# Kernel tuning notes

Hardware: AMD Instinct MI355X
Metric: run time of the kernel (lower is better)

## Reference

```python
import jax, jax.numpy as jnp
import numpy as np

B, T, F, H1, H2 = 16384, 10, 500, 256, 100  # batch, seq_len, noise_dim/seq_len, LSTM units, GRU units


def setup_inputs() -> dict:
    key = jax.random.key(0)
    ks = jax.random.split(key, 10)
    s = 0.02  # small init so relu activations stay bounded over time steps
    return {
        "noise": jax.random.normal(ks[0], (B, T * F), dtype=jnp.float32),
        "Wx_lstm": jax.random.normal(ks[1], (F, 4 * H1), dtype=jnp.float32) * s,
        "Wh_lstm": jax.random.normal(ks[2], (H1, 4 * H1), dtype=jnp.float32) * s,
        "b_lstm": jnp.zeros((4 * H1,), dtype=jnp.float32),
        "Wx_gru": jax.random.normal(ks[3], (H1, 3 * H2), dtype=jnp.float32) * s,
        "Wh_gru": jax.random.normal(ks[4], (H2, 3 * H2), dtype=jnp.float32) * s,
        "b_in_gru": jnp.zeros((3 * H2,), dtype=jnp.float32),
        "b_rec_gru": jnp.zeros((3 * H2,), dtype=jnp.float32),
        "Wd": jax.random.normal(ks[5], (H2, T), dtype=jnp.float32) * s,
        "bd": jnp.zeros((T,), dtype=jnp.float32),
    }


def _lstm(x, Wx, Wh, b):
    # x: [T, B, F]; Keras LSTM with activation='relu', recurrent_activation='sigmoid'
    Bn = x.shape[1]
    H = Wh.shape[0]
    def step(carry, x_t):
        h, c = carry
        z = x_t @ Wx + h @ Wh + b  # [B, 4H]
        i, f, g, o = jnp.split(z, 4, axis=-1)  # Keras gate order: i, f, c, o
        i = jax.nn.sigmoid(i)
        f = jax.nn.sigmoid(f)
        g = jax.nn.relu(g)
        o = jax.nn.sigmoid(o)
        c = f * c + i * g
        h = o * jax.nn.relu(c)
        return (h, c), h
    h0 = jnp.zeros((Bn, H), dtype=x.dtype)
    (_, _), hs = jax.lax.scan(step, (h0, h0), x)
    return hs  # [T, B, H]


def _gru(x, Wx, Wh, b_in, b_rec):
    # x: [T, B, H1]; Keras GRU (reset_after=True) with activation='relu'
    Bn = x.shape[1]
    H = Wh.shape[0]
    def step(h, x_t):
        mx = x_t @ Wx + b_in    # [B, 3H]
        mh = h @ Wh + b_rec     # [B, 3H]
        xz, xr, xh = jnp.split(mx, 3, axis=-1)  # Keras gate order: z, r, h
        hz, hr, hh = jnp.split(mh, 3, axis=-1)
        z = jax.nn.sigmoid(xz + hz)
        r = jax.nn.sigmoid(xr + hr)
        hcand = jax.nn.relu(xh + r * hh)
        h = z * h + (1.0 - z) * hcand
        return h, None
    h0 = jnp.zeros((Bn, H), dtype=x.dtype)
    h_final, _ = jax.lax.scan(step, h0, x)
    return h_final  # [B, H]


def reference(noise, Wx_lstm, Wh_lstm, b_lstm, Wx_gru, Wh_gru, b_in_gru, b_rec_gru, Wd, bd):
    Fdim = Wx_lstm.shape[0]
    Tdim = noise.shape[1] // Fdim
    x = noise.reshape(noise.shape[0], Tdim, Fdim)      # Reshape((T, F))
    x = jnp.transpose(x, (1, 0, 2))                    # [T, B, F] for scan
    hs = _lstm(x, Wx_lstm, Wh_lstm, b_lstm)            # [T, B, 256]
    h = _gru(hs, Wx_gru, Wh_gru, b_in_gru, b_rec_gru)  # [B, 100]
    return jax.nn.relu(h @ Wd + bd)                    # [B, T]
```

## Files before the change

### kernel.cpp

```cpp
#include <hip/hip_runtime.h>

#define Bsz 16384
#define TT 10
#define FF 500
#define H1c 256
#define H2c 100

typedef _Float16 half8 __attribute__((ext_vector_type(8)));
typedef float floatx4 __attribute__((ext_vector_type(4)));

__device__ __forceinline__ float sigm(float x) { return 1.0f / (1.0f + __expf(-x)); }

#define GLOAD16(g, l) __builtin_amdgcn_global_load_lds( \
    (const __attribute__((address_space(1))) void*)(g), \
    (__attribute__((address_space(3))) void*)(l), 16, 0, 0)

__global__ __launch_bounds__(256)
void conv_all(const float* __restrict__ noise, _Float16* __restrict__ xc)
{
    const int idx = blockIdx.x * 256 + threadIdx.x;
    const int rb = idx >> 6;
    const int kc = (idx & 63) << 3;
    const int b = rb / 10;
    const int t = rb - b * 10;
    const float* src = noise + (size_t)rb * FF + kc;
    half8 v;
    if (kc + 8 <= FF) {
        float4 u0 = *(const float4*)src;
        float4 u1 = *(const float4*)(src + 4);
        v[0] = (_Float16)u0.x; v[1] = (_Float16)u0.y; v[2] = (_Float16)u0.z; v[3] = (_Float16)u0.w;
        v[4] = (_Float16)u1.x; v[5] = (_Float16)u1.y; v[6] = (_Float16)u1.z; v[7] = (_Float16)u1.w;
    } else {
        #pragma unroll
        for (int j = 0; j < 8; ++j)
            v[j] = (kc + j < FF) ? (_Float16)src[j] : (_Float16)0.f;
    }
    *(half8*)(xc + ((size_t)t * Bsz + b) * 512 + kc) = v;
}

__global__ __launch_bounds__(256)
void prep_lstm_w(const float* __restrict__ Wx, const float* __restrict__ Wh,
                 _Float16* __restrict__ WT)
{
    const int idx = blockIdx.x * 256 + threadIdx.x;
    const int np = idx / 768, k = idx % 768;
    const int A2 = np >> 8, B2 = (np >> 6) & 3, g = (np >> 4) & 3, u = np & 15;
    const int U = A2 * 64 + B2 * 16 + u;
    const int col = g * 256 + U;
    float v = 0.f;
    if (k < 512) { if (k < FF) v = Wx[(size_t)k * 1024 + col]; }
    else v = Wh[(size_t)(k - 512) * 1024 + col];
    WT[idx] = (_Float16)v;
}

__global__ __launch_bounds__(256)
void prep_gru_w(const float* __restrict__ Wxg, const float* __restrict__ Whg,
                _Float16* __restrict__ WT)
{
    const int idx = blockIdx.x * 256 + threadIdx.x;
    if (idx >= 384 * 384) return;
    const int np = idx / 384, k = idx % 384;
    const int nb = np / 96, rem = np % 96;
    const int wxx = rem / 48, g = (rem % 48) / 16, u = rem & 15;
    const int U = nb * 32 + wxx * 16 + u;
    float v = 0.f;
    if (U < H2c) {
        if (k < 256) v = Wxg[(size_t)k * 300 + g * H2c + U];
        else if (k - 256 < H2c) v = Whg[(size_t)(k - 256) * 300 + g * H2c + U];
    }
    WT[idx] = (_Float16)v;
}

__device__ __forceinline__
void lstm_tile(int bid, const _Float16* __restrict__ xct, const _Float16* __restrict__ WT,
               const float* __restrict__ bias,
               const _Float16* __restrict__ h_prev, const float* __restrict__ c_prev,
               _Float16* __restrict__ h_out, float* __restrict__ c_out,
               int first, _Float16* smem)
{
    _Float16* As = smem;
    _Float16* Bs = smem + 32768;

    const int tid = threadIdx.x;
    const int lane = tid & 63;
    const int w = tid >> 6;
    const int wy = w >> 2, wx = w & 3;
    const int xcd = bid & 7;
    const int nb = xcd >> 1;
    const int row0 = (((xcd & 1) << 5) + (bid >> 3)) * 256;

    const int fr = lane & 15;
    const int l4 = lane >> 4;
    const int sr8 = lane >> 3;
    const int qsrc = (((lane & 7) ^ (sr8 & 7)) << 3);

    floatx4 acc[8][4];
    #pragma unroll
    for (int a = 0; a < 8; ++a)
        #pragma unroll
        for (int b = 0; b < 4; ++b) acc[a][b] = (floatx4){0.f, 0.f, 0.f, 0.f};

    const int nkt = first ? 8 : 12;

    #pragma unroll
    for (int q = 0; q < 4; ++q) {
        const int r = q * 64 + w * 8;
        GLOAD16(xct + (size_t)(row0 + r + sr8) * 512 + qsrc, &As[r * 64]);
        GLOAD16(WT + (size_t)(nb * 256 + r + sr8) * 768 + qsrc, &Bs[r * 64]);
    }
    __syncthreads();

    for (int T = 0; T < nkt; ++T) {
        const int pbase = (T & 1) * 16384;
        const int sbase = pbase ^ 16384;
        const int kb2 = (T + 1) * 64;
        const bool do_stage = (T + 1 < nkt);
        const bool from_x = kb2 < 512;

        half8 af[4][2], bf[2][2];

        auto LOAD_AF = [&](int mh) {
            #pragma unroll
            for (int j = 0; j < 4; ++j) {
                const int row = wy * 128 + (mh * 4 + j) * 16 + fr;
                #pragma unroll
                for (int ks = 0; ks < 2; ++ks) {
                    const int ch = (ks * 4 + l4) ^ (fr & 7);
                    af[j][ks] = *(const half8*)&As[pbase + row * 64 + ch * 8];
                }
            }
        };
        auto LOAD_BF = [&](int nh) {
            #pragma unroll
            for (int jn = 0; jn < 2; ++jn) {
                const int row = wx * 64 + (nh * 2 + jn) * 16 + fr;
                #pragma unroll
                for (int ks = 0; ks < 2; ++ks) {
                    const int ch = (ks * 4 + l4) ^ (fr & 7);
                    bf[jn][ks] = *(const half8*)&Bs[pbase + row * 64 + ch * 8];
                }
            }
        };
        auto STAGE_Q = [&](int q) {
            const int r = q * 64 + w * 8;
            if (from_x)
                GLOAD16(xct + (size_t)(row0 + r + sr8) * 512 + kb2 + qsrc, &As[sbase + r * 64]);
            else
                GLOAD16(h_prev + (size_t)(row0 + r + sr8) * 256 + (kb2 - 512) + qsrc, &As[sbase + r * 64]);
            GLOAD16(WT + (size_t)(nb * 256 + r + sr8) * 768 + kb2 + qsrc, &Bs[sbase + r * 64]);
        };
        auto MFMA_Q = [&](int mh, int nh) {
            __builtin_amdgcn_s_setprio(1);
            #pragma unroll
            for (int ks = 0; ks < 2; ++ks)
                #pragma unroll
                for (int j = 0; j < 4; ++j)
                    #pragma unroll
                    for (int jn = 0; jn < 2; ++jn)
                        acc[mh * 4 + j][nh * 2 + jn] = __builtin_amdgcn_mfma_f32_16x16x32_f16(
                            af[j][ks], bf[jn][ks], acc[mh * 4 + j][nh * 2 + jn], 0, 0, 0);
            __builtin_amdgcn_s_setprio(0);
        };

        LOAD_AF(0); LOAD_BF(0);
        if (do_stage) { STAGE_Q(0); STAGE_Q(1); }
        MFMA_Q(0, 0);
        LOAD_BF(1);
        if (do_stage) { STAGE_Q(2); STAGE_Q(3); }
        MFMA_Q(0, 1);
        LOAD_AF(1);
        MFMA_Q(1, 1);
        LOAD_BF(0);
        MFMA_Q(1, 0);
        __syncthreads();
    }

    const int U = nb * 64 + wx * 16 + fr;
    const float bi = bias[0 * 256 + U];
    const float bff = bias[1 * 256 + U];
    const float bg = bias[2 * 256 + U];
    const float bo = bias[3 * 256 + U];
    const int rbase = row0 + wy * 128 + l4 * 4;
    #pragma unroll
    for (int mi = 0; mi < 8; ++mi) {
        #pragma unroll
        for (int r = 0; r < 4; ++r) {
            const int row = rbase + mi * 16 + r;
            const float cp = first ? 0.f : c_prev[(size_t)row * 256 + U];
            const float zi = acc[mi][0][r] + bi;
            const float zf = acc[mi][1][r] + bff;
            const float zg = acc[mi][2][r] + bg;
            const float zo = acc[mi][3][r] + bo;
            const float ig = sigm(zi), fg = sigm(zf), og = sigm(zo);
            const float gg = fmaxf(zg, 0.f);
            const float cv = fg * cp + ig * gg;
            const float hv = og * fmaxf(cv, 0.f);
            c_out[(size_t)row * 256 + U] = cv;
            h_out[(size_t)row * 256 + U] = (_Float16)hv;
        }
    }
}

__device__ __forceinline__
void gru_tile(int bid, int first,
              const _Float16* __restrict__ h_r, const _Float16* __restrict__ g16_r,
              const _Float16* __restrict__ WTg,
              const float* __restrict__ b_in, const float* __restrict__ b_rec,
              _Float16* __restrict__ g16_w,
              _Float16* As, _Float16* Bs)
{
    const int tid = threadIdx.x;
    const int lane = tid & 63;
    const int w = tid >> 6;
    const int wq = w >> 2;
    const int wn = w & 3;
    const int rb0 = bid * 64;
    const int fr = lane & 15;
    const int l4 = lane >> 4;
    const int sr8 = lane >> 3;
    const int qsrc = (((lane & 7) ^ sr8) << 3);

    floatx4 accA[2][6], accB[2][6];
    #pragma unroll
    for (int a = 0; a < 2; ++a)
        #pragma unroll
        for (int b = 0; b < 6; ++b) {
            accA[a][b] = (floatx4){0.f, 0.f, 0.f, 0.f};
            accB[a][b] = (floatx4){0.f, 0.f, 0.f, 0.f};
        }

    const int nkt = first ? 4 : 6;
    for (int kt = 0; kt < nkt; ++kt) {
        const int kb = kt * 64;
        {
            const int r = w * 8;
            if (kt < 4)
                GLOAD16(h_r + (size_t)(rb0 + r + sr8) * 256 + kb + qsrc, &As[r * 64]);
            else
                GLOAD16(g16_r + (size_t)(rb0 + r + sr8) * 128 + (kb - 256) + qsrc, &As[r * 64]);
        }
        #pragma unroll
        for (int q = 0; q < 6; ++q) {
            const int r = q * 64 + w * 8;
            GLOAD16(WTg + (size_t)(r + sr8) * 384 + kb + qsrc, &Bs[r * 64]);
        }
        __syncthreads();
        #pragma unroll
        for (int ks = 0; ks < 2; ++ks) {
            half8 af[2], bf[6];
            const int ch0 = (ks * 4 + l4) ^ (fr & 7);
            #pragma unroll
            for (int mf = 0; mf < 2; ++mf) {
                const int row = wq * 32 + mf * 16 + fr;
                af[mf] = *(const half8*)&As[row * 64 + ch0 * 8];
            }
            #pragma unroll
            for (int nf = 0; nf < 6; ++nf) {
                const int row = wn * 96 + nf * 16 + fr;
                bf[nf] = *(const half8*)&Bs[row * 64 + ch0 * 8];
            }
            if (kt < 4) {
                #pragma unroll
                for (int mf = 0; mf < 2; ++mf)
                    #pragma unroll
                    for (int nf = 0; nf < 6; ++nf)
                        accA[mf][nf] = __builtin_amdgcn_mfma_f32_16x16x32_f16(af[mf], bf[nf], accA[mf][nf], 0, 0, 0);
            } else {
                #pragma unroll
                for (int mf = 0; mf < 2; ++mf)
                    #pragma unroll
                    for (int nf = 0; nf < 6; ++nf)
                        accB[mf][nf] = __builtin_amdgcn_mfma_f32_16x16x32_f16(af[mf], bf[nf], accB[mf][nf], 0, 0, 0);
            }
        }
        __syncthreads();
    }

    #pragma unroll
    for (int mf = 0; mf < 2; ++mf) {
        #pragma unroll
        for (int wxx = 0; wxx < 2; ++wxx) {
            const int U = wn * 32 + wxx * 16 + fr;
            const bool uv = U < H2c;
            const float bzi = uv ? b_in[U] : 0.f;
            const float bri = uv ? b_in[H2c + U] : 0.f;
            const float bhi = uv ? b_in[2 * H2c + U] : 0.f;
            const float bzr = uv ? b_rec[U] : 0.f;
            const float brr = uv ? b_rec[H2c + U] : 0.f;
            const float bhr = uv ? b_rec[2 * H2c + U] : 0.f;
            const int nf0 = wxx * 3;
            #pragma unroll
            for (int r = 0; r < 4; ++r) {
                const int row = rb0 + wq * 32 + mf * 16 + l4 * 4 + r;
                const float gp = (!first && uv) ? (float)g16_r[(size_t)row * 128 + U] : 0.f;
                const float mxz = accA[mf][nf0 + 0][r] + bzi;
                const float mxr = accA[mf][nf0 + 1][r] + bri;
                const float mxh = accA[mf][nf0 + 2][r] + bhi;
                const float mhz = accB[mf][nf0 + 0][r] + bzr;
                const float mhr = accB[mf][nf0 + 1][r] + brr;
                const float mhh = accB[mf][nf0 + 2][r] + bhr;
                const float z = sigm(mxz + mhz);
                const float rr = sigm(mxr + mhr);
                const float hc = fmaxf(mxh + rr * mhh, 0.f);
                const float g = z * gp + (1.f - z) * hc;
                g16_w[(size_t)row * 128 + U] = uv ? (_Float16)g : (_Float16)0.f;
            }
        }
    }
}

__device__ __forceinline__
void dense_tile(int bid, const _Float16* __restrict__ hg, const float* __restrict__ Wd,
                const float* __restrict__ bd, float* __restrict__ out)
{
    const int tid = threadIdx.x;
    if (tid < 64) {
        const int row = bid * 64 + tid;
        float acc[TT];
        #pragma unroll
        for (int j = 0; j < TT; ++j) acc[j] = 0.f;
        const _Float16* gr = hg + (size_t)row * 128;
        for (int k = 0; k < H2c; ++k) {
            const float xv = (float)gr[k];
            #pragma unroll
            for (int j = 0; j < TT; ++j) acc[j] += xv * Wd[k * TT + j];
        }
        #pragma unroll
        for (int j = 0; j < TT; ++j)
            out[(size_t)row * TT + j] = fmaxf(acc[j] + bd[j], 0.f);
    }
}

__global__ __launch_bounds__(512, 2)
void step_fused(const _Float16* __restrict__ xct, const _Float16* __restrict__ WTl,
                const float* __restrict__ b_l,
                const _Float16* __restrict__ h_prev, const float* __restrict__ c_prev,
                _Float16* __restrict__ h_out, float* __restrict__ c_out,
                const _Float16* __restrict__ WTg,
                const float* __restrict__ b_in, const float* __restrict__ b_rec,
                const _Float16* __restrict__ g16_r, _Float16* __restrict__ g16_w,
                int lstm_first, int gru_on, int gru_first)
{
    extern __shared__ _Float16 smem[];
    const int bid = blockIdx.x;
    lstm_tile(bid, xct, WTl, b_l, h_prev, c_prev, h_out, c_out, lstm_first, smem);
    if (gru_on)
        gru_tile(bid, gru_first, h_prev, g16_r, WTg, b_in, b_rec, g16_w,
                 smem, smem + 32768);
}

__global__ __launch_bounds__(512, 2)
void gru_dense_tail(const _Float16* __restrict__ h_r, const _Float16* __restrict__ g16_r,
                    const _Float16* __restrict__ WTg,
                    const float* __restrict__ b_in, const float* __restrict__ b_rec,
                    _Float16* __restrict__ g16_w,
                    const float* __restrict__ Wd, const float* __restrict__ bd,
                    float* __restrict__ out)
{
    __shared__ _Float16 smem[28672];
    gru_tile(blockIdx.x, 0, h_r, g16_r, WTg, b_in, b_rec, g16_w,
             smem, smem + 4096);
    __syncthreads();
    dense_tile(blockIdx.x, g16_w, Wd, bd, out);
}

extern "C" void kernel_launch(void* const* d_in, const int* in_sizes, int n_in,
                              void* d_out, int out_size, void* d_ws, size_t ws_size,
                              hipStream_t stream)
{
    const float* noise  = (const float*)d_in[0];
    const float* Wx_l   = (const float*)d_in[1];
    const float* Wh_l   = (const float*)d_in[2];
    const float* b_l    = (const float*)d_in[3];
    const float* Wx_g   = (const float*)d_in[4];
    const float* Wh_g   = (const float*)d_in[5];
    const float* b_in   = (const float*)d_in[6];
    const float* b_rec  = (const float*)d_in[7];
    const float* Wd     = (const float*)d_in[8];
    const float* bd     = (const float*)d_in[9];
    float* outf = (float*)d_out;

    char* p = (char*)d_ws;
    auto alloc = [&](size_t bytes) {
        char* r = p;
        p += (bytes + 255) & ~(size_t)255;
        return r;
    };
    _Float16* WTl  = (_Float16*)alloc((size_t)1024 * 768 * 2);
    _Float16* WTg  = (_Float16*)alloc((size_t)384 * 384 * 2);
    _Float16* xc   = (_Float16*)alloc((size_t)Bsz * TT * 512 * 2);
    _Float16* h16A = (_Float16*)alloc((size_t)Bsz * 256 * 2);
    _Float16* h16B = (_Float16*)alloc((size_t)Bsz * 256 * 2);
    float*    cA   = (float*)alloc((size_t)Bsz * 256 * 4);
    float*    cB   = (float*)alloc((size_t)Bsz * 256 * 4);
    _Float16* g16A = (_Float16*)alloc((size_t)Bsz * 128 * 2);
    _Float16* g16B = (_Float16*)alloc((size_t)Bsz * 128 * 2);

    (void)hipFuncSetAttribute((const void*)step_fused,
                              hipFuncAttributeMaxDynamicSharedMemorySize, 131072);

    conv_all<<<Bsz * TT * 64 / 256, 256, 0, stream>>>(noise, xc);
    prep_lstm_w<<<1024 * 768 / 256, 256, 0, stream>>>(Wx_l, Wh_l, WTl);
    prep_gru_w<<<(384 * 384 + 255) / 256, 256, 0, stream>>>(Wx_g, Wh_g, WTg);

    _Float16* hb[2] = {h16A, h16B};
    float*    cb[2] = {cA, cB};
    _Float16* gh[2] = {g16A, g16B};

    for (int t = 0; t < TT; ++t) {
        const int wi = t & 1, ri = (t + 1) & 1;
        step_fused<<<256, 512, 131072, stream>>>(
            xc + (size_t)t * Bsz * 512, WTl, b_l,
            hb[ri], cb[ri], hb[wi], cb[wi],
            WTg, b_in, b_rec, gh[wi], gh[ri],
            t == 0 ? 1 : 0, t >= 1 ? 1 : 0, t == 1 ? 1 : 0);
    }
    gru_dense_tail<<<256, 512, 0, stream>>>(hb[1], gh[0], WTg, b_in, b_rec,
                                            gh[1], Wd, bd, outf);
}
```

Baseline: 559.9 us.

## Overlap per-timestep input fp16 conversion with recurrent step kernels

The upfront conversion of all ten noise timesteps to fp16 is replaced by converting only plane 0 before the loop. Each step kernel launches 64 extra blocks that convert the next timestep's input plane while the 256 LSTM/GRU blocks work, hiding the conversion bandwidth behind compute. The risk is that the extra blocks, each needing 128KB of dynamic shared memory, compete for CU slots and memory bandwidth with the recurrent tiles and may delay them.

```diff
diff --git a/kernel.cpp b/kernel.cpp
--- a/kernel.cpp
+++ b/kernel.cpp
@@ -15,15 +15,13 @@
     (const __attribute__((address_space(1))) void*)(g), \
     (__attribute__((address_space(3))) void*)(l), 16, 0, 0)
 
-__global__ __launch_bounds__(256)
-void conv_all(const float* __restrict__ noise, _Float16* __restrict__ xc)
-{
-    const int idx = blockIdx.x * 256 + threadIdx.x;
-    const int rb = idx >> 6;
-    const int kc = (idx & 63) << 3;
-    const int b = rb / 10;
-    const int t = rb - b * 10;
-    const float* src = noise + (size_t)rb * FF + kc;
+__device__ __forceinline__
+void conv_chunks(const float* __restrict__ noise, _Float16* __restrict__ xc,
+                 int tp, int gidx)
+{
+    const int b = gidx >> 6;
+    const int kc = (gidx & 63) << 3;
+    const float* src = noise + (size_t)b * (TT * FF) + tp * FF + kc;
     half8 v;
     if (kc + 8 <= FF) {
         float4 u0 = *(const float4*)src;
@@ -35,7 +33,13 @@
         for (int j = 0; j < 8; ++j)
             v[j] = (kc + j < FF) ? (_Float16)src[j] : (_Float16)0.f;
     }
-    *(half8*)(xc + ((size_t)t * Bsz + b) * 512 + kc) = v;
+    *(half8*)(xc + ((size_t)tp * Bsz + b) * 512 + kc) = v;
+}
+
+__global__ __launch_bounds__(256)
+void conv_plane0(const float* __restrict__ noise, _Float16* __restrict__ xc)
+{
+    conv_chunks(noise, xc, 0, blockIdx.x * 256 + threadIdx.x);
 }
 
 __global__ __launch_bounds__(256)
@@ -339,14 +343,22 @@
                 const _Float16* __restrict__ WTg,
                 const float* __restrict__ b_in, const float* __restrict__ b_rec,
                 const _Float16* __restrict__ g16_r, _Float16* __restrict__ g16_w,
-                int lstm_first, int gru_on, int gru_first)
+                const float* __restrict__ noise, _Float16* __restrict__ xc_all,
+                int lstm_first, int gru_on, int gru_first, int conv_plane)
 {
     extern __shared__ _Float16 smem[];
     const int bid = blockIdx.x;
-    lstm_tile(bid, xct, WTl, b_l, h_prev, c_prev, h_out, c_out, lstm_first, smem);
-    if (gru_on)
-        gru_tile(bid, gru_first, h_prev, g16_r, WTg, b_in, b_rec, g16_w,
-                 smem, smem + 32768);
+    if (bid < 256) {
+        lstm_tile(bid, xct, WTl, b_l, h_prev, c_prev, h_out, c_out, lstm_first, smem);
+        if (gru_on)
+            gru_tile(bid, gru_first, h_prev, g16_r, WTg, b_in, b_rec, g16_w,
+                     smem, smem + 32768);
+    } else if (conv_plane > 0) {
+        const int base = (bid - 256) * 512 + threadIdx.x;
+        #pragma unroll
+        for (int j = 0; j < 32; ++j)
+            conv_chunks(noise, xc_all, conv_plane, base + j * 32768);
+    }
 }
 
 __global__ __launch_bounds__(512, 2)
@@ -399,7 +411,7 @@
     (void)hipFuncSetAttribute((const void*)step_fused,
                               hipFuncAttributeMaxDynamicSharedMemorySize, 131072);
 
-    conv_all<<<Bsz * TT * 64 / 256, 256, 0, stream>>>(noise, xc);
+    conv_plane0<<<Bsz * 64 / 256, 256, 0, stream>>>(noise, xc);
     prep_lstm_w<<<1024 * 768 / 256, 256, 0, stream>>>(Wx_l, Wh_l, WTl);
     prep_gru_w<<<(384 * 384 + 255) / 256, 256, 0, stream>>>(Wx_g, Wh_g, WTg);
 
@@ -409,11 +421,14 @@
 
     for (int t = 0; t < TT; ++t) {
         const int wi = t & 1, ri = (t + 1) & 1;
-        step_fused<<<256, 512, 131072, stream>>>(
+        const int cp = (t + 1 < TT) ? t + 1 : 0;
+        const int grid = (cp > 0) ? 320 : 256;
+        step_fused<<<grid, 512, 131072, stream>>>(
             xc + (size_t)t * Bsz * 512, WTl, b_l,
             hb[ri], cb[ri], hb[wi], cb[wi],
             WTg, b_in, b_rec, gh[wi], gh[ri],
-            t == 0 ? 1 : 0, t >= 1 ? 1 : 0, t == 1 ? 1 : 0);
+            noise, xc,
+            t == 0 ? 1 : 0, t >= 1 ? 1 : 0, t == 1 ? 1 : 0, cp);
     }
     gru_dense_tail<<<256, 512, 0, stream>>>(hb[1], gh[0], WTg, b_in, b_rec,
                                             gh[1], Wd, bd, outf);
```

New measurement: 894.2 us. 59.7% more time.

## Hoist LSTM input projection into one batched GEMM over all timesteps

Applied to the files above, without the earlier changes.

Splits the LSTM weight into input and recurrent parts and computes x_t·Wx for all ten timesteps in a single large GEMM kernel up front, storing the gate pre-activations in fp16. Each per-step recurrent kernel then only runs the 256-wide h·Wh GEMM and adds the precomputed pre-activations in its epilogue. This shrinks the serial per-step work and lets the input projection run with full-grid parallelism. The cost is a large extra fp16 buffer written and read back through memory, and extra rounding from storing the pre-activations in fp16.

```diff
diff --git a/kernel.cpp b/kernel.cpp
--- a/kernel.cpp
+++ b/kernel.cpp
@@ -7,6 +7,7 @@
 #define H2c 100
 
 typedef _Float16 half8 __attribute__((ext_vector_type(8)));
+typedef _Float16 half4 __attribute__((ext_vector_type(4)));
 typedef float floatx4 __attribute__((ext_vector_type(4)));
 
 __device__ __forceinline__ float sigm(float x) { return 1.0f / (1.0f + __expf(-x)); }
@@ -40,17 +41,19 @@
 
 __global__ __launch_bounds__(256)
 void prep_lstm_w(const float* __restrict__ Wx, const float* __restrict__ Wh,
-                 _Float16* __restrict__ WT)
+                 _Float16* __restrict__ WTx, _Float16* __restrict__ WTh)
 {
     const int idx = blockIdx.x * 256 + threadIdx.x;
     const int np = idx / 768, k = idx % 768;
     const int A2 = np >> 8, B2 = (np >> 6) & 3, g = (np >> 4) & 3, u = np & 15;
     const int U = A2 * 64 + B2 * 16 + u;
     const int col = g * 256 + U;
-    float v = 0.f;
-    if (k < 512) { if (k < FF) v = Wx[(size_t)k * 1024 + col]; }
-    else v = Wh[(size_t)(k - 512) * 1024 + col];
-    WT[idx] = (_Float16)v;
+    if (k < 512) {
+        float v = (k < FF) ? Wx[(size_t)k * 1024 + col] : 0.f;
+        WTx[(size_t)np * 512 + k] = (_Float16)v;
+    } else {
+        WTh[(size_t)np * 256 + (k - 512)] = (_Float16)Wh[(size_t)(k - 512) * 1024 + col];
+    }
 }
 
 __global__ __launch_bounds__(256)
@@ -71,13 +74,11 @@
     WT[idx] = (_Float16)v;
 }
 
-__device__ __forceinline__
-void lstm_tile(int bid, const _Float16* __restrict__ xct, const _Float16* __restrict__ WT,
-               const float* __restrict__ bias,
-               const _Float16* __restrict__ h_prev, const float* __restrict__ c_prev,
-               _Float16* __restrict__ h_out, float* __restrict__ c_out,
-               int first, _Float16* smem)
-{
+__global__ __launch_bounds__(512, 2)
+void big_zx(const _Float16* __restrict__ xc, const _Float16* __restrict__ WTx,
+            _Float16* __restrict__ ZX)
+{
+    extern __shared__ _Float16 smem[];
     _Float16* As = smem;
     _Float16* Bs = smem + 32768;
 
@@ -85,9 +86,11 @@
     const int lane = tid & 63;
     const int w = tid >> 6;
     const int wy = w >> 2, wx = w & 3;
+    const int bid = blockIdx.x;
     const int xcd = bid & 7;
-    const int nb = xcd >> 1;
-    const int row0 = (((xcd & 1) << 5) + (bid >> 3)) * 256;
+    const int i = bid >> 3;
+    const int nb = i & 3;
+    const int row0 = (xcd * 80 + (i >> 2)) * 256;
 
     const int fr = lane & 15;
     const int l4 = lane >> 4;
@@ -100,25 +103,21 @@
         #pragma unroll
         for (int b = 0; b < 4; ++b) acc[a][b] = (floatx4){0.f, 0.f, 0.f, 0.f};
 
-    const int nkt = first ? 8 : 12;
-
     #pragma unroll
     for (int q = 0; q < 4; ++q) {
         const int r = q * 64 + w * 8;
-        GLOAD16(xct + (size_t)(row0 + r + sr8) * 512 + qsrc, &As[r * 64]);
-        GLOAD16(WT + (size_t)(nb * 256 + r + sr8) * 768 + qsrc, &Bs[r * 64]);
+        GLOAD16(xc + (size_t)(row0 + r + sr8) * 512 + qsrc, &As[r * 64]);
+        GLOAD16(WTx + (size_t)(nb * 256 + r + sr8) * 512 + qsrc, &Bs[r * 64]);
     }
     __syncthreads();
 
-    for (int T = 0; T < nkt; ++T) {
+    for (int T = 0; T < 8; ++T) {
         const int pbase = (T & 1) * 16384;
         const int sbase = pbase ^ 16384;
         const int kb2 = (T + 1) * 64;
-        const bool do_stage = (T + 1 < nkt);
-        const bool from_x = kb2 < 512;
+        const bool do_stage = (T + 1 < 8);
 
         half8 af[4][2], bf[2][2];
-
         auto LOAD_AF = [&](int mh) {
             #pragma unroll
             for (int j = 0; j < 4; ++j) {
@@ -143,11 +142,8 @@
         };
         auto STAGE_Q = [&](int q) {
             const int r = q * 64 + w * 8;
-            if (from_x)
-                GLOAD16(xct + (size_t)(row0 + r + sr8) * 512 + kb2 + qsrc, &As[sbase + r * 64]);
-            else
-                GLOAD16(h_prev + (size_t)(row0 + r + sr8) * 256 + (kb2 - 512) + qsrc, &As[sbase + r * 64]);
-            GLOAD16(WT + (size_t)(nb * 256 + r + sr8) * 768 + kb2 + qsrc, &Bs[sbase + r * 64]);
+            GLOAD16(xc + (size_t)(row0 + r + sr8) * 512 + kb2 + qsrc, &As[sbase + r * 64]);
+            GLOAD16(WTx + (size_t)(nb * 256 + r + sr8) * 512 + kb2 + qsrc, &Bs[sbase + r * 64]);
         };
         auto MFMA_Q = [&](int mh, int nh) {
             __builtin_amdgcn_s_setprio(1);
@@ -175,22 +171,140 @@
         __syncthreads();
     }
 
+    const size_t cb = nb * 256 + wx * 64 + fr * 4;
+    const int rbase = row0 + wy * 128 + l4 * 4;
+    #pragma unroll
+    for (int mi = 0; mi < 8; ++mi) {
+        #pragma unroll
+        for (int r = 0; r < 4; ++r) {
+            const int row = rbase + mi * 16 + r;
+            half4 v;
+            v[0] = (_Float16)acc[mi][0][r];
+            v[1] = (_Float16)acc[mi][1][r];
+            v[2] = (_Float16)acc[mi][2][r];
+            v[3] = (_Float16)acc[mi][3][r];
+            *(half4*)(ZX + (size_t)row * 1024 + cb) = v;
+        }
+    }
+}
+
+__device__ __forceinline__
+void lstm_rec_tile(int bid, const _Float16* __restrict__ zx,
+                   const _Float16* __restrict__ WTh, const float* __restrict__ bias,
+                   const _Float16* __restrict__ h_prev, const float* __restrict__ c_prev,
+                   _Float16* __restrict__ h_out, float* __restrict__ c_out,
+                   int first, _Float16* smem)
+{
+    _Float16* As = smem;
+    _Float16* Bs = smem + 32768;
+
+    const int tid = threadIdx.x;
+    const int lane = tid & 63;
+    const int w = tid >> 6;
+    const int wy = w >> 2, wx = w & 3;
+    const int xcd = bid & 7;
+    const int nb = xcd >> 1;
+    const int row0 = (((xcd & 1) << 5) + (bid >> 3)) * 256;
+
+    const int fr = lane & 15;
+    const int l4 = lane >> 4;
+    const int sr8 = lane >> 3;
+    const int qsrc = (((lane & 7) ^ (sr8 & 7)) << 3);
+
+    floatx4 acc[8][4];
+    #pragma unroll
+    for (int a = 0; a < 8; ++a)
+        #pragma unroll
+        for (int b = 0; b < 4; ++b) acc[a][b] = (floatx4){0.f, 0.f, 0.f, 0.f};
+
+    if (!first) {
+        #pragma unroll
+        for (int q = 0; q < 4; ++q) {
+            const int r = q * 64 + w * 8;
+            GLOAD16(h_prev + (size_t)(row0 + r + sr8) * 256 + qsrc, &As[r * 64]);
+            GLOAD16(WTh + (size_t)(nb * 256 + r + sr8) * 256 + qsrc, &Bs[r * 64]);
+        }
+        __syncthreads();
+
+        for (int T = 0; T < 4; ++T) {
+            const int pbase = (T & 1) * 16384;
+            const int sbase = pbase ^ 16384;
+            const int kb2 = (T + 1) * 64;
+            const bool do_stage = (T + 1 < 4);
+
+            half8 af[4][2], bf[2][2];
+            auto LOAD_AF = [&](int mh) {
+                #pragma unroll
+                for (int j = 0; j < 4; ++j) {
+                    const int row = wy * 128 + (mh * 4 + j) * 16 + fr;
+                    #pragma unroll
+                    for (int ks = 0; ks < 2; ++ks) {
+                        const int ch = (ks * 4 + l4) ^ (fr & 7);
+                        af[j][ks] = *(const half8*)&As[pbase + row * 64 + ch * 8];
+                    }
+                }
+            };
+            auto LOAD_BF = [&](int nh) {
+                #pragma unroll
+                for (int jn = 0; jn < 2; ++jn) {
+                    const int row = wx * 64 + (nh * 2 + jn) * 16 + fr;
+                    #pragma unroll
+                    for (int ks = 0; ks < 2; ++ks) {
+                        const int ch = (ks * 4 + l4) ^ (fr & 7);
+                        bf[jn][ks] = *(const half8*)&Bs[pbase + row * 64 + ch * 8];
+                    }
+                }
+            };
+            auto STAGE_Q = [&](int q) {
+                const int r = q * 64 + w * 8;
+                GLOAD16(h_prev + (size_t)(row0 + r + sr8) * 256 + kb2 + qsrc, &As[sbase + r * 64]);
+                GLOAD16(WTh + (size_t)(nb * 256 + r + sr8) * 256 + kb2 + qsrc, &Bs[sbase + r * 64]);
+            };
+            auto MFMA_Q = [&](int mh, int nh) {
+                __builtin_amdgcn_s_setprio(1);
+                #pragma unroll
+                for (int ks = 0; ks < 2; ++ks)
+                    #pragma unroll
+                    for (int j = 0; j < 4; ++j)
+                        #pragma unroll
+                        for (int jn = 0; jn < 2; ++jn)
+                            acc[mh * 4 + j][nh * 2 + jn] = __builtin_amdgcn_mfma_f32_16x16x32_f16(
+                                af[j][ks], bf[jn][ks], acc[mh * 4 + j][nh * 2 + jn], 0, 0, 0);
+                __builtin_amdgcn_s_setprio(0);
+            };
+
+            LOAD_AF(0); LOAD_BF(0);
+            if (do_stage) { STAGE_Q(0); STAGE_Q(1); }
+            MFMA_Q(0, 0);
+            LOAD_BF(1);
+            if (do_stage) { STAGE_Q(2); STAGE_Q(3); }
+            MFMA_Q(0, 1);
+            LOAD_AF(1);
+            MFMA_Q(1, 1);
+            LOAD_BF(0);
+            MFMA_Q(1, 0);
+            __syncthreads();
+        }
+    }
+
     const int U = nb * 64 + wx * 16 + fr;
     const float bi = bias[0 * 256 + U];
     const float bff = bias[1 * 256 + U];
     const float bg = bias[2 * 256 + U];
     const float bo = bias[3 * 256 + U];
+    const size_t cb = nb * 256 + wx * 64 + fr * 4;
     const int rbase = row0 + wy * 128 + l4 * 4;
     #pragma unroll
     for (int mi = 0; mi < 8; ++mi) {
         #pragma unroll
         for (int r = 0; r < 4; ++r) {
             const int row = rbase + mi * 16 + r;
+            half4 zx4 = *(const half4*)(zx + (size_t)row * 1024 + cb);
             const float cp = first ? 0.f : c_prev[(size_t)row * 256 + U];
-            const float zi = acc[mi][0][r] + bi;
-            const float zf = acc[mi][1][r] + bff;
-            const float zg = acc[mi][2][r] + bg;
-            const float zo = acc[mi][3][r] + bo;
+            const float zi = acc[mi][0][r] + (float)zx4[0] + bi;
+            const float zf = acc[mi][1][r] + (float)zx4[1] + bff;
+            const float zg = acc[mi][2][r] + (float)zx4[2] + bg;
+            const float zo = acc[mi][3][r] + (float)zx4[3] + bo;
             const float ig = sigm(zi), fg = sigm(zf), og = sigm(zo);
             const float gg = fmaxf(zg, 0.f);
             const float cv = fg * cp + ig * gg;
@@ -332,18 +446,18 @@
 }
 
 __global__ __launch_bounds__(512, 2)
-void step_fused(const _Float16* __restrict__ xct, const _Float16* __restrict__ WTl,
-                const float* __restrict__ b_l,
-                const _Float16* __restrict__ h_prev, const float* __restrict__ c_prev,
-                _Float16* __restrict__ h_out, float* __restrict__ c_out,
-                const _Float16* __restrict__ WTg,
-                const float* __restrict__ b_in, const float* __restrict__ b_rec,
-                const _Float16* __restrict__ g16_r, _Float16* __restrict__ g16_w,
-                int lstm_first, int gru_on, int gru_first)
+void rec_fused(const _Float16* __restrict__ zx, const _Float16* __restrict__ WTh,
+               const float* __restrict__ b_l,
+               const _Float16* __restrict__ h_prev, const float* __restrict__ c_prev,
+               _Float16* __restrict__ h_out, float* __restrict__ c_out,
+               const _Float16* __restrict__ WTg,
+               const float* __restrict__ b_in, const float* __restrict__ b_rec,
+               const _Float16* __restrict__ g16_r, _Float16* __restrict__ g16_w,
+               int lstm_first, int gru_on, int gru_first)
 {
     extern __shared__ _Float16 smem[];
     const int bid = blockIdx.x;
-    lstm_tile(bid, xct, WTl, b_l, h_prev, c_prev, h_out, c_out, lstm_first, smem);
+    lstm_rec_tile(bid, zx, WTh, b_l, h_prev, c_prev, h_out, c_out, lstm_first, smem);
     if (gru_on)
         gru_tile(bid, gru_first, h_prev, g16_r, WTg, b_in, b_rec, g16_w,
                  smem, smem + 32768);
@@ -386,9 +500,11 @@
         p += (bytes + 255) & ~(size_t)255;
         return r;
     };
-    _Float16* WTl  = (_Float16*)alloc((size_t)1024 * 768 * 2);
+    _Float16* WTx  = (_Float16*)alloc((size_t)1024 * 512 * 2);
+    _Float16* WTh  = (_Float16*)alloc((size_t)1024 * 256 * 2);
     _Float16* WTg  = (_Float16*)alloc((size_t)384 * 384 * 2);
     _Float16* xc   = (_Float16*)alloc((size_t)Bsz * TT * 512 * 2);
+    _Float16* ZX   = (_Float16*)alloc((size_t)Bsz * TT * 1024 * 2);
     _Float16* h16A = (_Float16*)alloc((size_t)Bsz * 256 * 2);
     _Float16* h16B = (_Float16*)alloc((size_t)Bsz * 256 * 2);
     float*    cA   = (float*)alloc((size_t)Bsz * 256 * 4);
@@ -396,12 +512,15 @@
     _Float16* g16A = (_Float16*)alloc((size_t)Bsz * 128 * 2);
     _Float16* g16B = (_Float16*)alloc((size_t)Bsz * 128 * 2);
 
-    (void)hipFuncSetAttribute((const void*)step_fused,
+    (void)hipFuncSetAttribute((const void*)big_zx,
                               hipFuncAttributeMaxDynamicSharedMemorySize, 131072);
+    (void)hipFuncSetAttribute((const void*)rec_fused,
+                              hipFuncAttributeMaxDynamicSharedMemorySize, 131072);
 
     conv_all<<<Bsz * TT * 64 / 256, 256, 0, stream>>>(noise, xc);
-    prep_lstm_w<<<1024 * 768 / 256, 256, 0, stream>>>(Wx_l, Wh_l, WTl);
+    prep_lstm_w<<<1024 * 768 / 256, 256, 0, stream>>>(Wx_l, Wh_l, WTx, WTh);
     prep_gru_w<<<(384 * 384 + 255) / 256, 256, 0, stream>>>(Wx_g, Wh_g, WTg);
+    big_zx<<<2560, 512, 131072, stream>>>(xc, WTx, ZX);
 
     _Float16* hb[2] = {h16A, h16B};
     float*    cb[2] = {cA, cB};
@@ -409,8 +528,8 @@
 
     for (int t = 0; t < TT; ++t) {
         const int wi = t & 1, ri = (t + 1) & 1;
-        step_fused<<<256, 512, 131072, stream>>>(
-            xc + (size_t)t * Bsz * 512, WTl, b_l,
+        rec_fused<<<256, 512, 131072, stream>>>(
+            ZX + (size_t)t * Bsz * 1024, WTh, b_l,
             hb[ri], cb[ri], hb[wi], cb[wi],
             WTg, b_in, b_rec, gh[wi], gh[ri],
             t == 0 ? 1 : 0, t >= 1 ? 1 : 0, t == 1 ? 1 : 0);
```

Result: slower. 754.7 us (+34.8%).
